# Kernel optimization log

Hardware: AMD Instinct MI355X
Metric: run time of the kernel (lower is better)

Reference implementation:

```python
import jax, jax.numpy as jnp
import numpy as np

B, S, D, H, NH, C = 32, 512, 768, 768, 4, 10
HD = H // NH


def _lin(x, w, b):
    return x @ w.T + b


def _ln(x, g, b, eps=1e-5):
    mu = jnp.mean(x, axis=-1, keepdims=True)
    var = jnp.mean(jnp.square(x - mu), axis=-1, keepdims=True)
    return (x - mu) * jax.lax.rsqrt(var + eps) * g + b


def setup_inputs() -> dict:
    key = jax.random.key(0)
    ks = jax.random.split(key, 16)
    w = lambda k, shape: jax.random.normal(k, shape, dtype=jnp.float32) * 0.02
    return {
        "x": jax.random.normal(ks[0], (B, S, D), dtype=jnp.float32),
        "wq": w(ks[1], (H, D)), "bq": jnp.zeros((H,), jnp.float32),
        "wk": w(ks[2], (H, D)), "bk": jnp.zeros((H,), jnp.float32),
        "wv": w(ks[3], (H, D)), "bv": jnp.zeros((H,), jnp.float32),
        "wx": w(ks[4], (H, D)), "bx": jnp.zeros((H,), jnp.float32),
        "in_proj_w": w(ks[5], (3 * H, H)), "in_proj_b": jnp.zeros((3 * H,), jnp.float32),
        "out_proj_w": w(ks[6], (H, H)), "out_proj_b": jnp.zeros((H,), jnp.float32),
        "fc1a_w": w(ks[7], (H, H)), "fc1a_b": jnp.zeros((H,), jnp.float32),
        "fc1b_w": w(ks[8], (H, H)), "fc1b_b": jnp.zeros((H,), jnp.float32),
        "ln_g": jnp.ones((H,), jnp.float32), "ln_b": jnp.zeros((H,), jnp.float32),
        "fc2_w": w(ks[9], (C, H)), "fc2_b": jnp.zeros((C,), jnp.float32),
    }


def reference(x, wq, bq, wk, bk, wv, bv, wx, bx, in_proj_w, in_proj_b,
              out_proj_w, out_proj_b, fc1a_w, fc1a_b, fc1b_w, fc1b_b,
              ln_g, ln_b, fc2_w, fc2_b):
    # Vectorized sinusoidal PE matching the triple loop:
    # even i: sin(pos / 10000^(2i/D)); odd i: cos(pos / 10000^(2(i-1)/D))
    d = x.shape[2]
    pos = jnp.arange(x.shape[1], dtype=x.dtype)[:, None]          # [S,1]
    i = jnp.arange(d)
    i_even = (i - (i % 2)).astype(x.dtype)                        # 2*(i - i%2)/d exponent
    angle = pos / jnp.power(jnp.asarray(10000.0, x.dtype), 2.0 * i_even / d)  # [S,D]
    pe = jnp.where(i % 2 == 0, jnp.sin(angle), jnp.cos(angle))
    x = x + pe[None]

    q = _lin(x, wq, bq)
    k = _lin(x, wk, bk)
    v = _lin(x, wv, bv)
    xr = _lin(x, wx, bx)

    # torch MultiheadAttention: in_proj, split heads, SDPA, out_proj
    wq_i, wk_i, wv_i = jnp.split(in_proj_w, 3, axis=0)
    bq_i, bk_i, bv_i = jnp.split(in_proj_b, 3, axis=0)
    b = x.shape[0]
    q2 = _lin(q, wq_i, bq_i).reshape(b, -1, NH, HD)
    k2 = _lin(k, wk_i, bk_i).reshape(b, -1, NH, HD)
    v2 = _lin(v, wv_i, bv_i).reshape(b, -1, NH, HD)
    scores = jnp.einsum('bqhd,bkhd->bhqk', q2, k2) / jnp.sqrt(jnp.asarray(HD, x.dtype))
    attn = jax.nn.softmax(scores, axis=-1)
    ctx = jnp.einsum('bhqk,bkhd->bqhd', attn, v2).reshape(b, -1, H)
    attn_out = _lin(ctx, out_proj_w, out_proj_b)

    x = _ln(xr + attn_out, ln_g, ln_b)
    ffn = _lin(jax.nn.relu(_lin(x, fc1a_w, fc1a_b)), fc1b_w, fc1b_b)
    x = _ln(x + ffn, ln_g, ln_b)
    x = jnp.sum(x, axis=1)
    return _lin(x, fc2_w, fc2_b)
```

## Files before the change

kernel.cpp:

```cpp
#include <hip/hip_runtime.h>
#include <hip/hip_bf16.h>

typedef __bf16 bf16;
typedef __bf16 bf16x8 __attribute__((ext_vector_type(8)));
typedef __bf16 bf16x4 __attribute__((ext_vector_type(4)));
typedef __bf16 bf16x2 __attribute__((ext_vector_type(2)));
typedef float  f32x4  __attribute__((ext_vector_type(4)));

#define GLD16(g, l) __builtin_amdgcn_global_load_lds(                        \
    (const __attribute__((address_space(1))) void*)(g),                      \
    (__attribute__((address_space(3))) void*)(l), 16, 0, 0)

template<int BM, int BN, int MFR, int NFR>
__global__ __launch_bounds__(256, 3)
void gemm_nt(const bf16* __restrict__ A, const bf16* __restrict__ B,
             bf16* __restrict__ C, const float* __restrict__ bias,
             int K, int lda, int ldb, int ldc,
             int inner,
             long long aOut, long long aIn,
             long long bOut, long long bIn,
             long long cOut, long long cIn,
             float alpha, int relu,
             const bf16* __restrict__ res, int ldr)
{
    const int z  = blockIdx.z;
    const int zo = z / inner;
    const int zi = z - zo * inner;
    A += (long long)zo * aOut + (long long)zi * aIn;
    B += (long long)zo * bOut + (long long)zi * bIn;
    C += (long long)zo * cOut + (long long)zi * cIn;

    const int tm = blockIdx.y * BM;
    const int tn = blockIdx.x * BN;

    __shared__ __align__(16) bf16 smem[(BM + BN) * 64];
    bf16* As = smem;
    bf16* Bs = smem + BM * 64;

    const int tid  = threadIdx.x;
    const int lane = tid & 63;
    const int wid  = tid >> 6;
    const int wr   = wid >> 1;
    const int wc   = wid & 1;

    f32x4 acc[MFR][NFR];
#pragma unroll
    for (int i = 0; i < MFR; ++i)
#pragma unroll
        for (int j = 0; j < NFR; ++j) acc[i][j] = (f32x4){0.f, 0.f, 0.f, 0.f};

    const int srow = lane >> 3;
    const int gch8 = ((lane & 7) ^ srow) * 8;

    const int NA = BM / 32;
    const int NB = BN / 32;

    const bf16* aP[NA];
#pragma unroll
    for (int jj = 0; jj < NA; ++jj) {
        const int R0 = (wid * NA + jj) * 8;
        aP[jj] = A + (long long)(tm + R0 + srow) * lda + gch8;
    }
    const bf16* bP[NB];
#pragma unroll
    for (int jj = 0; jj < NB; ++jj) {
        const int R0 = (wid * NB + jj) * 8;
        bP[jj] = B + (long long)(tn + R0 + srow) * ldb + gch8;
    }

    const int lr = lane & 15;
    const int qg = lane >> 4;

    for (int kt = 0; kt < K; kt += 64) {
#pragma unroll
        for (int jj = 0; jj < NA; ++jj)
            GLD16(aP[jj], As + (wid * NA + jj) * 512);
#pragma unroll
        for (int jj = 0; jj < NB; ++jj)
            GLD16(bP[jj], Bs + (wid * NB + jj) * 512);
        __syncthreads();

#pragma unroll
        for (int h = 0; h < 2; ++h) {
            const int off = ((qg + h * 4) ^ (lr & 7)) * 8;
            bf16x8 af[MFR], bfr[NFR];
#pragma unroll
            for (int i = 0; i < MFR; ++i)
                af[i] = *(const bf16x8*)(As + (wr * MFR * 16 + i * 16 + lr) * 64 + off);
#pragma unroll
            for (int j = 0; j < NFR; ++j)
                bfr[j] = *(const bf16x8*)(Bs + (wc * NFR * 16 + j * 16 + lr) * 64 + off);
#pragma unroll
            for (int i = 0; i < MFR; ++i)
#pragma unroll
                for (int j = 0; j < NFR; ++j)
                    acc[i][j] = __builtin_amdgcn_mfma_f32_16x16x32_bf16(
                        af[i], bfr[j], acc[i][j], 0, 0, 0);
        }
        __syncthreads();
#pragma unroll
        for (int jj = 0; jj < NA; ++jj) aP[jj] += 64;
#pragma unroll
        for (int jj = 0; jj < NB; ++jj) bP[jj] += 64;
    }

#pragma unroll
    for (int i = 0; i < MFR; ++i) {
#pragma unroll
        for (int j = 0; j < NFR; ++j) {
            const int mm0 = tm + wr * MFR * 16 + i * 16 + (lane >> 4) * 4;
            const int nn  = tn + wc * NFR * 16 + j * 16 + (lane & 15);
#pragma unroll
            for (int r = 0; r < 4; ++r) {
                float v = acc[i][j][r] * alpha;
                if (bias) v += bias[nn];
                if (res)  v += (float)res[(long long)(mm0 + r) * ldr + nn];
                if (relu) v = fmaxf(v, 0.f);
                C[(long long)(mm0 + r) * ldc + nn] = (bf16)v;
            }
        }
    }
}

#define BAR8()  __builtin_amdgcn_s_barrier()
#define LGKM0() do { asm volatile("s_waitcnt lgkmcnt(0)" ::: "memory");      \
                     __builtin_amdgcn_sched_barrier(0); } while (0)

#define RD_A(S, MB)                                                          \
    _Pragma("unroll") for (int mi = 0; mi < 4; ++mi)                         \
    _Pragma("unroll") for (int h = 0; h < 2; ++h)                            \
        af[mi][h] = *(const bf16x8*)((S) + aBase + ((MB) + mi) * 1024 +      \
                                     (h ? koff1 : koff0));

#define RD_B(S, NJ)                                                          \
    _Pragma("unroll") for (int h = 0; h < 2; ++h)                            \
        bfv[NJ][h] = *(const bf16x8*)((S) + bBase + (NJ) * 1024 +            \
                                      (h ? koff1 : koff0));

#define MFMA_Q(MB, N0, N1)                                                   \
    __builtin_amdgcn_s_setprio(1);                                          \
    _Pragma("unroll") for (int h = 0; h < 2; ++h)                            \
    _Pragma("unroll") for (int mi = 0; mi < 4; ++mi) {                       \
        acc[(MB)+mi][(N0)] = __builtin_amdgcn_mfma_f32_16x16x32_bf16(        \
            af[mi][h], bfv[(N0)][h], acc[(MB)+mi][(N0)], 0, 0, 0);           \
        acc[(MB)+mi][(N1)] = __builtin_amdgcn_mfma_f32_16x16x32_bf16(        \
            af[mi][h], bfv[(N1)][h], acc[(MB)+mi][(N1)], 0, 0, 0);           \
    }                                                                        \
    __builtin_amdgcn_s_setprio(0);

#define STAGE_A(DST)                                                         \
    _Pragma("unroll") for (int jj = 0; jj < 4; ++jj) {                       \
        GLD16(aP[jj], (DST) + (wid * 4 + jj) * 512);  aP[jj] += 64; }

#define STAGE_B(DST)                                                         \
    _Pragma("unroll") for (int jj = 0; jj < 4; ++jj) {                       \
        GLD16(bP[jj], (DST) + 16384 + (wid * 4 + jj) * 512);  bP[jj] += 64; }

#define K_TILE_F(CUR, NXT, STG, LAST)                                        \
  {                                                                          \
    RD_A((CUR), 0); RD_B((CUR), 0); RD_B((CUR), 1);                          \
    if (STG) { STAGE_A(NXT) }                                                \
    LGKM0();                                                                 \
    MFMA_Q(0, 0, 1)                                                          \
    RD_B((CUR), 2); RD_B((CUR), 3);                                          \
    if (STG) { STAGE_B(NXT) }                                                \
    LGKM0();                                                                 \
    MFMA_Q(0, 2, 3)                                                          \
    RD_A((CUR), 4);                                                          \
    LGKM0();                                                                 \
    MFMA_Q(4, 2, 3)                                                          \
    MFMA_Q(4, 0, 1)                                                          \
    if (!(LAST)) { asm volatile("s_waitcnt vmcnt(0)" ::: "memory");          \
                   __builtin_amdgcn_sched_barrier(0); BAR8(); }              \
  }

__global__ __launch_bounds__(512, 2)
void gemm_qkv_8ph(const bf16* __restrict__ A, const bf16* __restrict__ B,
                  bf16* __restrict__ C, const float* __restrict__ bias)
{
    constexpr int LDA = 768, LDB = 768, LDC = 3072;
    const int tm = blockIdx.y * 256;
    const int tn = blockIdx.x * 256;

    __shared__ __align__(16) bf16 smem[2][2 * 256 * 64];

    const int tid  = threadIdx.x;
    const int lane = tid & 63;
    const int wid  = tid >> 6;
    const int wr   = wid >> 2;
    const int wc   = wid & 3;
    const int lr   = lane & 15;
    const int qg   = lane >> 4;

    const int srow = lane >> 3;
    const int gch8 = ((lane & 7) ^ srow) * 8;
    const bf16* aP[4];
    const bf16* bP[4];
#pragma unroll
    for (int jj = 0; jj < 4; ++jj) {
        aP[jj] = A + (long long)(tm + wid * 32 + jj * 8 + srow) * LDA + gch8;
        bP[jj] = B + (long long)(tn + wid * 32 + jj * 8 + srow) * LDB + gch8;
    }

    f32x4 acc[8][4];
#pragma unroll
    for (int i = 0; i < 8; ++i)
#pragma unroll
        for (int j = 0; j < 4; ++j) acc[i][j] = (f32x4){0.f, 0.f, 0.f, 0.f};

    const int aBase = (wr * 128 + lr) * 64;
    const int bBase = 16384 + (wc * 64 + lr) * 64;
    const int koff0 = ((qg    ) ^ (lr & 7)) * 8;
    const int koff1 = ((qg + 4) ^ (lr & 7)) * 8;

    bf16x8 af[4][2];
    bf16x8 bfv[4][2];

    bf16* S0 = &smem[0][0];
    bf16* S1 = &smem[1][0];

    STAGE_A(S0)
    STAGE_B(S0)
    asm volatile("s_waitcnt vmcnt(0)" ::: "memory");
    BAR8();

#pragma unroll 1
    for (int it = 0; it < 5; ++it) {
        K_TILE_F(S0, S1, 1, 0)
        K_TILE_F(S1, S0, 1, 0)
    }
    K_TILE_F(S0, S1, 1, 0)
    K_TILE_F(S1, S0, 0, 1)

    float bv[4];
#pragma unroll
    for (int j = 0; j < 4; ++j) bv[j] = bias[tn + wc * 64 + j * 16 + lr];

#pragma unroll
    for (int i = 0; i < 8; ++i) {
        const int mm0 = tm + wr * 128 + i * 16 + qg * 4;
#pragma unroll
        for (int j = 0; j < 4; ++j) {
            const int nn = tn + wc * 64 + j * 16 + lr;
#pragma unroll
            for (int r = 0; r < 4; ++r)
                C[(long long)(mm0 + r) * LDC + nn] = (bf16)(acc[i][j][r] + bv[j]);
        }
    }
}

__global__ __launch_bounds__(512, 2)
void gemm_flow(const bf16* __restrict__ A, const bf16* __restrict__ B,
               bf16* __restrict__ C, const float* __restrict__ bias,
               int lda, int ldb, int ldc, int relu,
               const bf16* __restrict__ res, int ldr)
{
    const int tm = blockIdx.y * 256;
    const int tn = blockIdx.x * 256;

    __shared__ __align__(16) bf16 smem[2][2 * 256 * 64];

    const int tid  = threadIdx.x;
    const int lane = tid & 63;
    const int wid  = tid >> 6;
    const int wr   = wid >> 2;
    const int wc   = wid & 3;
    const int lr   = lane & 15;
    const int qg   = lane >> 4;

    const int srow = lane >> 3;
    const int gch8 = ((lane & 7) ^ srow) * 8;
    const bf16* aP[4];
    const bf16* bP[4];
#pragma unroll
    for (int jj = 0; jj < 4; ++jj) {
        aP[jj] = A + (long long)(tm + wid * 32 + jj * 8 + srow) * lda + gch8;
        bP[jj] = B + (long long)(tn + wid * 32 + jj * 8 + srow) * ldb + gch8;
    }

    f32x4 acc[8][4];
#pragma unroll
    for (int i = 0; i < 8; ++i)
#pragma unroll
        for (int j = 0; j < 4; ++j) acc[i][j] = (f32x4){0.f, 0.f, 0.f, 0.f};

    const int aBase = (wr * 128 + lr) * 64;
    const int bBase = 16384 + (wc * 64 + lr) * 64;
    const int koff0 = ((qg    ) ^ (lr & 7)) * 8;
    const int koff1 = ((qg + 4) ^ (lr & 7)) * 8;

    bf16x8 af[4][2];
    bf16x8 bfv[4][2];

    bf16* S0 = &smem[0][0];
    bf16* S1 = &smem[1][0];

    STAGE_A(S0)
    STAGE_B(S0)
    asm volatile("s_waitcnt vmcnt(0)" ::: "memory");
    BAR8();

#pragma unroll 1
    for (int it = 0; it < 5; ++it) {
        K_TILE_F(S0, S1, 1, 0)
        K_TILE_F(S1, S0, 1, 0)
    }
    K_TILE_F(S0, S1, 1, 0)
    K_TILE_F(S1, S0, 0, 1)

    float bv[4];
#pragma unroll
    for (int j = 0; j < 4; ++j) bv[j] = bias ? bias[tn + wc * 64 + j * 16 + lr] : 0.f;

#pragma unroll
    for (int i = 0; i < 8; ++i) {
        const int mm0 = tm + wr * 128 + i * 16 + qg * 4;
#pragma unroll
        for (int j = 0; j < 4; ++j) {
            const int nn = tn + wc * 64 + j * 16 + lr;
#pragma unroll
            for (int r = 0; r < 4; ++r) {
                float v = acc[i][j][r] + bv[j];
                if (res)  v += (float)res[(long long)(mm0 + r) * ldr + nn];
                if (relu) v = fmaxf(v, 0.f);
                C[(long long)(mm0 + r) * ldc + nn] = (bf16)v;
            }
        }
    }
}

__global__ __launch_bounds__(256, 2)
void fused_attn_kernel(bf16* __restrict__ qkvx)
{
    const int flat = blockIdx.x;
    const int qt = (flat >> 3) & 3;
    const int z  = (flat & 7) | ((flat >> 5) << 3);
    const int b  = z >> 2, h = z & 3;

    const bf16* Qg = qkvx + (long long)b * 512 * 3072 + h * 192;
    const bf16* Kg = Qg + 768;
    const bf16* Vg = Qg + 1536;

    __shared__ __align__(16) bf16 Ks[64 * 192];
    __shared__ __align__(16) bf16 VTs[192 * 64];
    __shared__ __align__(16) bf16 Pb[4 * 32 * 64];

    const int tid  = threadIdx.x;
    const int lane = tid & 63;
    const int wid  = tid >> 6;
    const int lr   = lane & 15;
    const int qg   = lane >> 4;
    const int m0   = qt * 128 + wid * 32;

    bf16x8 qf[2][6];
#pragma unroll
    for (int mt = 0; mt < 2; ++mt)
#pragma unroll
        for (int t = 0; t < 6; ++t)
            qf[mt][t] = *(const bf16x8*)(Qg + (long long)(m0 + mt * 16 + lr) * 3072
                                         + t * 32 + qg * 8);

    const bf16* kP[6];
#pragma unroll
    for (int i = 0; i < 6; ++i) {
        const int c = i * 256 + tid;
        const int krow = c / 24, kcc = c % 24;
        const int kgc  = (kcc & 24) | ((kcc & 7) ^ (krow & 7));
        kP[i] = Kg + (long long)krow * 3072 + kgc * 8;
    }
    const int vkp = tid & 31;
    const int vdc = tid >> 5;

    f32x4 acc[2][12];
#pragma unroll
    for (int mt = 0; mt < 2; ++mt)
#pragma unroll
        for (int dt = 0; dt < 12; ++dt) acc[mt][dt] = (f32x4){0.f, 0.f, 0.f, 0.f};
    float mrow[2][4], lrow[2][4];
#pragma unroll
    for (int mt = 0; mt < 2; ++mt)
#pragma unroll
        for (int r = 0; r < 4; ++r) { mrow[mt][r] = -3e38f; lrow[mt][r] = 0.f; }

    const float alpha = 0.0721687836f;

    for (int kt = 0; kt < 8; ++kt) {
#pragma unroll
        for (int i = 0; i < 6; ++i)
            GLD16(kP[i], Ks + (i * 256 + wid * 64) * 8);
#pragma unroll
        for (int i = 0; i < 3; ++i) {
            const int dc = vdc + i * 8;
            const bf16* p = Vg + (long long)(2 * vkp) * 3072 + dc * 8;
            const bf16x8 v0 = *(const bf16x8*)(p);
            const bf16x8 v1 = *(const bf16x8*)(p + 3072);
#pragma unroll
            for (int j = 0; j < 8; ++j) {
                const int d = dc * 8 + j;
                bf16x2 pk; pk[0] = v0[j]; pk[1] = v1[j];
                *(bf16x2*)(VTs + d * 64 + ((vkp >> 2) ^ (d & 7)) * 8
                           + 2 * (vkp & 3)) = pk;
            }
        }
        __syncthreads();

        f32x4 sf[2][4];
#pragma unroll
        for (int mt = 0; mt < 2; ++mt)
#pragma unroll
            for (int nt = 0; nt < 4; ++nt) sf[mt][nt] = (f32x4){0.f, 0.f, 0.f, 0.f};
#pragma unroll
        for (int nt = 0; nt < 4; ++nt) {
#pragma unroll
            for (int t = 0; t < 6; ++t) {
                const int ch = t * 4 + qg;
                const int ph = (ch & 24) | ((ch & 7) ^ (lr & 7));
                const bf16x8 kf = *(const bf16x8*)(Ks + (nt * 16 + lr) * 192 + ph * 8);
                sf[0][nt] = __builtin_amdgcn_mfma_f32_16x16x32_bf16(qf[0][t], kf, sf[0][nt], 0, 0, 0);
                sf[1][nt] = __builtin_amdgcn_mfma_f32_16x16x32_bf16(qf[1][t], kf, sf[1][nt], 0, 0, 0);
            }
        }

#pragma unroll
        for (int mt = 0; mt < 2; ++mt) {
            float mx[4], a[4], rs[4], p[4][4];
#pragma unroll
            for (int r = 0; r < 4; ++r) {
                float v0 = fmaxf(sf[mt][0][r], sf[mt][1][r]);
                float v1 = fmaxf(sf[mt][2][r], sf[mt][3][r]);
                mx[r] = fmaxf(v0, v1) * alpha;
            }
#pragma unroll
            for (int msk = 1; msk <= 8; msk <<= 1)
#pragma unroll
                for (int r = 0; r < 4; ++r) mx[r] = fmaxf(mx[r], __shfl_xor(mx[r], msk));
#pragma unroll
            for (int r = 0; r < 4; ++r) {
                const float mn = fmaxf(mrow[mt][r], mx[r]);
                a[r] = __expf(mrow[mt][r] - mn);
                mrow[mt][r] = mn;
                rs[r] = 0.f;
            }
#pragma unroll
            for (int nt = 0; nt < 4; ++nt)
#pragma unroll
                for (int r = 0; r < 4; ++r) {
                    p[nt][r] = __expf(sf[mt][nt][r] * alpha - mrow[mt][r]);
                    rs[r] += p[nt][r];
                }
#pragma unroll
            for (int msk = 1; msk <= 8; msk <<= 1)
#pragma unroll
                for (int r = 0; r < 4; ++r) rs[r] += __shfl_xor(rs[r], msk);
#pragma unroll
            for (int r = 0; r < 4; ++r) lrow[mt][r] = lrow[mt][r] * a[r] + rs[r];
#pragma unroll
            for (int dt = 0; dt < 12; ++dt)
#pragma unroll
                for (int r = 0; r < 4; ++r) acc[mt][dt][r] *= a[r];
#pragma unroll
            for (int nt = 0; nt < 4; ++nt)
#pragma unroll
                for (int r = 0; r < 4; ++r) {
                    const int row = mt * 16 + qg * 4 + r;
                    const int ph2 = (nt * 2 + (lr >> 3)) ^ (row & 7);
                    Pb[wid * 2048 + row * 64 + ph2 * 8 + (lr & 7)] = (bf16)p[nt][r];
                }
        }

        bf16x8 pf[2][2];
#pragma unroll
        for (int mt = 0; mt < 2; ++mt)
#pragma unroll
            for (int ks = 0; ks < 2; ++ks) {
                const int row = mt * 16 + lr;
                const int ph  = (ks * 4 + qg) ^ (lr & 7);
                pf[mt][ks] = *(const bf16x8*)(Pb + wid * 2048 + row * 64 + ph * 8);
            }
#pragma unroll
        for (int dt = 0; dt < 12; ++dt) {
#pragma unroll
            for (int ks = 0; ks < 2; ++ks) {
                const int ph = (ks * 4 + qg) ^ (lr & 7);
                const bf16x8 vf = *(const bf16x8*)(VTs + (dt * 16 + lr) * 64 + ph * 8);
                acc[0][dt] = __builtin_amdgcn_mfma_f32_16x16x32_bf16(pf[0][ks], vf, acc[0][dt], 0, 0, 0);
                acc[1][dt] = __builtin_amdgcn_mfma_f32_16x16x32_bf16(pf[1][ks], vf, acc[1][dt], 0, 0, 0);
            }
        }
        __syncthreads();
#pragma unroll
        for (int i = 0; i < 6; ++i) kP[i] += 64 * 3072;
        Vg += 64 * 3072;
    }

    bf16* Og = qkvx + (long long)b * 512 * 3072 + h * 192;
#pragma unroll
    for (int mt = 0; mt < 2; ++mt) {
        float inv[4];
#pragma unroll
        for (int r = 0; r < 4; ++r) inv[r] = 1.0f / lrow[mt][r];
#pragma unroll
        for (int dt = 0; dt < 12; ++dt)
#pragma unroll
            for (int r = 0; r < 4; ++r) {
                const int row = m0 + mt * 16 + qg * 4 + r;
                Og[(long long)row * 3072 + dt * 16 + lr] = (bf16)(acc[mt][dt][r] * inv[r]);
            }
    }
}

__device__ __forceinline__ void cast4(const float* src, bf16* dst, int i)
{
    const float4 v = *(const float4*)(src + (long long)i * 4);
    bf16x4 o;
    o[0] = (bf16)v.x; o[1] = (bf16)v.y; o[2] = (bf16)v.z; o[3] = (bf16)v.w;
    *(bf16x4*)(dst + (long long)i * 4) = o;
}

__global__ __launch_bounds__(256)
void prep_kernel(const float* __restrict__ wq, const float* __restrict__ wk,
                 const float* __restrict__ wv, const float* __restrict__ wx,
                 const float* __restrict__ inpw, const float* __restrict__ inpb,
                 const float* __restrict__ bq, const float* __restrict__ bk,
                 const float* __restrict__ bv, const float* __restrict__ bx,
                 const float* __restrict__ woutp, const float* __restrict__ wf1a,
                 const float* __restrict__ wf1b, const float* __restrict__ x,
                 bf16* __restrict__ WT3, bf16* __restrict__ INPJ,
                 bf16* __restrict__ WOUT, bf16* __restrict__ WF1A,
                 bf16* __restrict__ WF1B, bf16* __restrict__ WXD,
                 float* __restrict__ BCAT, bf16* __restrict__ XPE)
{
    const int blk = blockIdx.x;
    const int tid = threadIdx.x;
    __shared__ bf16 t[32][33];

    if (blk < 1728) {
        const int which = blk / 576, local = blk - which * 576;
        const float* src = (which == 0) ? wq : ((which == 1) ? wk : wv);
        bf16* dst = WT3 + (long long)which * 589824;
        const int r0 = (local / 24) * 32, c0 = (local % 24) * 32;
        const int tr = tid >> 5, tc = tid & 31;
#pragma unroll
        for (int k = 0; k < 4; ++k) {
            const int r = tr + k * 8;
            t[r][tc] = (bf16)src[(long long)(r0 + r) * 768 + c0 + tc];
        }
        __syncthreads();
#pragma unroll
        for (int k = 0; k < 4; ++k) {
            const int c = tr + k * 8;
            dst[(long long)(c0 + c) * 768 + r0 + tc] = t[tc][c];
        }
    } else if (blk < 3456) {
        cast4(inpw, INPJ, (blk - 1728) * 256 + tid);
    } else if (blk < 4032) {
        cast4(woutp, WOUT, (blk - 3456) * 256 + tid);
    } else if (blk < 4608) {
        cast4(wf1a, WF1A, (blk - 4032) * 256 + tid);
    } else if (blk < 5184) {
        cast4(wf1b, WF1B, (blk - 4608) * 256 + tid);
    } else if (blk < 5760) {
        cast4(wx, WXD, (blk - 5184) * 256 + tid);
    } else if (blk < 6051) {
        const int bl = blk - 5760;
        if (bl < 288) {
            const int g = tid >> 5, l = tid & 31;
            const int n = bl * 8 + g;
            const int zsec = n / 768;
            const float* bb = (zsec == 0) ? bq : ((zsec == 1) ? bk : bv);
            const float* wrow = inpw + (long long)n * 768;
            float s = 0.f;
            for (int d = l; d < 768; d += 32) s += wrow[d] * bb[d];
#pragma unroll
            for (int off = 16; off; off >>= 1) s += __shfl_xor(s, off);
            if (l == 0) BCAT[n] = inpb[n] + s;
        } else {
            const int n = (bl - 288) * 256 + tid;
            if (n < 768) BCAT[2304 + n] = bx[n];
        }
    } else {
        const int idx4 = ((blk - 6051) * 256 + tid) * 4;
        const int d    = idx4 % 768;
        const int row  = idx4 / 768;
        const int s    = row & 511;
        const float ksc = -0.034603417655076f;
        const float4 xv = *(const float4*)(x + (long long)idx4);
        float a0 = (float)s * exp2f((float)d * ksc);
        float a1 = (float)s * exp2f((float)(d + 2) * ksc);
        float s0, c0, s1, c1;
        sincosf(a0, &s0, &c0);
        sincosf(a1, &s1, &c1);
        bf16x4 o;
        o[0] = (bf16)(xv.x + s0);
        o[1] = (bf16)(xv.y + c0);
        o[2] = (bf16)(xv.z + s1);
        o[3] = (bf16)(xv.w + c1);
        *(bf16x4*)(XPE + (long long)idx4) = o;
    }
}

__global__ __launch_bounds__(192)
void ln1_kernel(const bf16* __restrict__ a, int lda_,
                bf16* __restrict__ o, int ldo,
                const float* __restrict__ g, const float* __restrict__ be)
{
    const int row = blockIdx.x;
    const int t   = threadIdx.x;
    const int d0  = t * 4;
    const bf16x4 av = *(const bf16x4*)(a + (long long)row * lda_ + d0);
    float xv[4];
#pragma unroll
    for (int k = 0; k < 4; ++k) xv[k] = (float)av[k];
    float s1 = xv[0] + xv[1] + xv[2] + xv[3];
    float s2 = xv[0]*xv[0] + xv[1]*xv[1] + xv[2]*xv[2] + xv[3]*xv[3];
    for (int off = 32; off; off >>= 1) {
        s1 += __shfl_xor(s1, off);
        s2 += __shfl_xor(s2, off);
    }
    __shared__ float red[6];
    const int wid = t >> 6, lane = t & 63;
    if (lane == 0) { red[wid] = s1; red[3 + wid] = s2; }
    __syncthreads();
    s1 = red[0] + red[1] + red[2];
    s2 = red[3] + red[4] + red[5];
    const float mu  = s1 * (1.0f / 768.0f);
    const float var = s2 * (1.0f / 768.0f) - mu * mu;
    const float rs  = rsqrtf(var + 1e-5f);
    const float4 gv = *(const float4*)(g + d0);
    const float4 ev = *(const float4*)(be + d0);
    bf16x4 ov;
    ov[0] = (bf16)(((xv[0] - mu) * rs) * gv.x + ev.x);
    ov[1] = (bf16)(((xv[1] - mu) * rs) * gv.y + ev.y);
    ov[2] = (bf16)(((xv[2] - mu) * rs) * gv.z + ev.z);
    ov[3] = (bf16)(((xv[3] - mu) * rs) * gv.w + ev.w);
    *(bf16x4*)(o + (long long)row * ldo + d0) = ov;
}

__global__ __launch_bounds__(256)
void ln2_reduce_kernel(const bf16* __restrict__ src,
                       const float* __restrict__ g, const float* __restrict__ be,
                       float* __restrict__ partial)
{
    const int blk  = blockIdx.x;
    const int tid  = threadIdx.x;
    const int wid  = tid >> 6, lane = tid & 63;
    const int d0   = lane * 12;

    float gv[12], ev[12];
#pragma unroll
    for (int k = 0; k < 12; k += 4) {
        *(float4*)(gv + k) = *(const float4*)(g + d0 + k);
        *(float4*)(ev + k) = *(const float4*)(be + d0 + k);
    }
    float acc[12];
#pragma unroll
    for (int k = 0; k < 12; ++k) acc[k] = 0.f;

    for (int i = 0; i < 8; ++i) {
        const int row = blk * 32 + i * 4 + wid;
        const bf16* p = src + (long long)row * 3072 + d0;
        float xv[12];
#pragma unroll
        for (int k = 0; k < 12; k += 4) {
            const bf16x4 v = *(const bf16x4*)(p + k);
            xv[k] = (float)v[0]; xv[k+1] = (float)v[1];
            xv[k+2] = (float)v[2]; xv[k+3] = (float)v[3];
        }
        float s1 = 0.f, s2 = 0.f;
#pragma unroll
        for (int k = 0; k < 12; ++k) { s1 += xv[k]; s2 += xv[k] * xv[k]; }
        for (int off = 32; off; off >>= 1) {
            s1 += __shfl_xor(s1, off);
            s2 += __shfl_xor(s2, off);
        }
        const float mu  = s1 * (1.0f / 768.0f);
        const float var = s2 * (1.0f / 768.0f) - mu * mu;
        const float rs  = rsqrtf(var + 1e-5f);
#pragma unroll
        for (int k = 0; k < 12; ++k) acc[k] += (xv[k] - mu) * rs * gv[k] + ev[k];
    }

    __shared__ float red[4][768];
#pragma unroll
    for (int k = 0; k < 12; k += 4)
        *(float4*)(&red[wid][d0 + k]) = *(const float4*)(acc + k);
    __syncthreads();
    if (wid == 0) {
#pragma unroll
        for (int k = 0; k < 12; k += 4) {
            const float4 a0 = *(const float4*)(&red[0][d0 + k]);
            const float4 a1 = *(const float4*)(&red[1][d0 + k]);
            const float4 a2 = *(const float4*)(&red[2][d0 + k]);
            const float4 a3 = *(const float4*)(&red[3][d0 + k]);
            *(float4*)(partial + (long long)blk * 768 + d0 + k) =
                make_float4(a0.x + a1.x + a2.x + a3.x, a0.y + a1.y + a2.y + a3.y,
                            a0.z + a1.z + a2.z + a3.z, a0.w + a1.w + a2.w + a3.w);
        }
    }
}

__global__ __launch_bounds__(192)
void reduce_fc2_stage2_kernel(const float* __restrict__ partial, const float* __restrict__ w,
                              const float* __restrict__ bias, float* __restrict__ out)
{
    const int b = blockIdx.x, t = threadIdx.x;
    const int d0 = t * 4;
    float a[4] = {0.f, 0.f, 0.f, 0.f};
    for (int c = 0; c < 16; ++c) {
        const float4 pv = *(const float4*)(partial + (long long)(b * 16 + c) * 768 + d0);
        a[0] += pv.x; a[1] += pv.y; a[2] += pv.z; a[3] += pv.w;
    }
    __shared__ float os[10];
    if (t < 10) os[t] = 0.f;
    __syncthreads();
    for (int c = 0; c < 10; ++c) {
        const float4 wv = *(const float4*)(w + c * 768 + d0);
        float p = wv.x * a[0] + wv.y * a[1] + wv.z * a[2] + wv.w * a[3];
        for (int off = 32; off; off >>= 1) p += __shfl_xor(p, off);
        if ((t & 63) == 0) atomicAdd(&os[c], p);
    }
    __syncthreads();
    if (t < 10) out[b * 10 + t] = os[t] + bias[t];
}

static const size_t OFF_XPE  = 0;
static const size_t OFF_WCAT = OFF_XPE  + (size_t)16384 * 768 * 2;
static const size_t OFF_WT3  = OFF_WCAT + (size_t)3072 * 768 * 2;
static const size_t OFF_INPJ = OFF_WT3  + (size_t)3 * 768 * 768 * 2;
static const size_t OFF_WOUT = OFF_INPJ + (size_t)2304 * 768 * 2;
static const size_t OFF_WF1A = OFF_WOUT + (size_t)768 * 768 * 2;
static const size_t OFF_WF1B = OFF_WF1A + (size_t)768 * 768 * 2;
static const size_t OFF_BCAT = OFF_WF1B + (size_t)768 * 768 * 2;
static const size_t OFF_QKVX = OFF_BCAT + (size_t)3072 * 4;
static const size_t OFF_VT   = OFF_QKVX + (size_t)16384 * 3072 * 2;
static const size_t OFF_S    = OFF_VT   + (size_t)128 * 192 * 512 * 2;
static const size_t OFF_X1   = OFF_S    + (size_t)128 * 512 * 512 * 2;

extern "C" void kernel_launch(void* const* d_in, const int* in_sizes, int n_in,
                              void* d_out, int out_size, void* d_ws, size_t ws_size,
                              hipStream_t stream)
{
    const float* x     = (const float*)d_in[0];
    const float* wq    = (const float*)d_in[1];
    const float* bq    = (const float*)d_in[2];
    const float* wk    = (const float*)d_in[3];
    const float* bk    = (const float*)d_in[4];
    const float* wv    = (const float*)d_in[5];
    const float* bv    = (const float*)d_in[6];
    const float* wx    = (const float*)d_in[7];
    const float* bx    = (const float*)d_in[8];
    const float* inpw  = (const float*)d_in[9];
    const float* inpb  = (const float*)d_in[10];
    const float* woutp = (const float*)d_in[11];
    const float* boutp = (const float*)d_in[12];
    const float* wf1a  = (const float*)d_in[13];
    const float* bf1a  = (const float*)d_in[14];
    const float* wf1b  = (const float*)d_in[15];
    const float* bf1b  = (const float*)d_in[16];
    const float* lng   = (const float*)d_in[17];
    const float* lnb   = (const float*)d_in[18];
    const float* wfc2  = (const float*)d_in[19];
    const float* bfc2  = (const float*)d_in[20];
    float* out = (float*)d_out;

    char* ws = (char*)d_ws;
    bf16*  XPE  = (bf16*)(ws + OFF_XPE);
    bf16*  WCAT = (bf16*)(ws + OFF_WCAT);
    bf16*  WT3  = (bf16*)(ws + OFF_WT3);
    bf16*  INPJ = (bf16*)(ws + OFF_INPJ);
    bf16*  WOUT = (bf16*)(ws + OFF_WOUT);
    bf16*  WF1A = (bf16*)(ws + OFF_WF1A);
    bf16*  WF1B = (bf16*)(ws + OFF_WF1B);
    float* BCAT = (float*)(ws + OFF_BCAT);
    bf16*  QKVX = (bf16*)(ws + OFF_QKVX);
    float* PART = (float*)(ws + OFF_S);
    bf16*  X1   = (bf16*)(ws + OFF_X1);

    prep_kernel<<<18339, 256, 0, stream>>>(wq, wk, wv, wx, inpw, inpb,
                                           bq, bk, bv, bx, woutp, wf1a, wf1b, x,
                                           WT3, INPJ, WOUT, WF1A, WF1B,
                                           WCAT + (size_t)2304 * 768, BCAT, XPE);

    gemm_nt<64, 128, 2, 4><<<dim3(6, 12, 3), 256, 0, stream>>>(
        INPJ, WT3, WCAT, nullptr, 768, 768, 768, 768,
        1, 589824, 0, 589824, 0, 589824, 0, 1.0f, 0, nullptr, 0);

    gemm_qkv_8ph<<<dim3(12, 64, 1), 512, 0, stream>>>(XPE, WCAT, QKVX, BCAT);

    fused_attn_kernel<<<512, 256, 0, stream>>>(QKVX);

    gemm_flow<<<dim3(3, 64, 1), 512, 0, stream>>>(
        QKVX, WOUT, QKVX + 768, boutp, 3072, 768, 3072,
        0, QKVX + 2304, 3072);

    ln1_kernel<<<16384, 192, 0, stream>>>(QKVX + 768, 3072, X1, 768, lng, lnb);

    gemm_flow<<<dim3(3, 64, 1), 512, 0, stream>>>(
        X1, WF1A, QKVX + 1536, bf1a, 768, 768, 3072,
        1, nullptr, 0);

    gemm_flow<<<dim3(3, 64, 1), 512, 0, stream>>>(
        QKVX + 1536, WF1B, QKVX + 2304, bf1b, 3072, 768, 3072,
        0, X1, 768);

    ln2_reduce_kernel<<<512, 256, 0, stream>>>(QKVX + 2304, lng, lnb, PART);

    reduce_fc2_stage2_kernel<<<32, 192, 0, stream>>>(PART, wfc2, bfc2, out);
}
```

Baseline: 455.2 us.

## Prefetch next K/V tiles into registers during attention compute

The attention kernel now loads the next K and V tiles from global memory into registers right after the barrier, so those loads overlap with the QK^T, softmax and PV MFMA work of the current tile. The direct global-to-LDS loads for K are replaced by register stores to LDS. Full __syncthreads are swapped for explicit lgkmcnt waits, raw barriers and sched_barriers so the compiler cannot sink the prefetch past the compute. The cost is more vector registers (kreg and vreg) on top of an already large accumulator set, which may lower occupancy or cause spills.

```diff
diff --git a/kernel.cpp b/kernel.cpp
--- a/kernel.cpp
+++ b/kernel.cpp
@@ -370,6 +370,18 @@
     }
     const int vkp = tid & 31;
     const int vdc = tid >> 5;
+    const bf16* vB = Vg + (long long)(2 * vkp) * 3072;
+
+    bf16x8 kreg[6];
+    bf16x8 vreg[3][2];
+#pragma unroll
+    for (int i = 0; i < 6; ++i) kreg[i] = *(const bf16x8*)kP[i];
+#pragma unroll
+    for (int i = 0; i < 3; ++i) {
+        const bf16* p = vB + (vdc + i * 8) * 8;
+        vreg[i][0] = *(const bf16x8*)(p);
+        vreg[i][1] = *(const bf16x8*)(p + 3072);
+    }
 
     f32x4 acc[2][12];
 #pragma unroll
@@ -387,22 +399,37 @@
     for (int kt = 0; kt < 8; ++kt) {
 #pragma unroll
         for (int i = 0; i < 6; ++i)
-            GLD16(kP[i], Ks + (i * 256 + wid * 64) * 8);
+            *(bf16x8*)(Ks + (i * 256 + wid * 64 + lane) * 8) = kreg[i];
 #pragma unroll
         for (int i = 0; i < 3; ++i) {
             const int dc = vdc + i * 8;
-            const bf16* p = Vg + (long long)(2 * vkp) * 3072 + dc * 8;
-            const bf16x8 v0 = *(const bf16x8*)(p);
-            const bf16x8 v1 = *(const bf16x8*)(p + 3072);
 #pragma unroll
             for (int j = 0; j < 8; ++j) {
                 const int d = dc * 8 + j;
-                bf16x2 pk; pk[0] = v0[j]; pk[1] = v1[j];
+                bf16x2 pk; pk[0] = vreg[i][0][j]; pk[1] = vreg[i][1][j];
                 *(bf16x2*)(VTs + d * 64 + ((vkp >> 2) ^ (d & 7)) * 8
                            + 2 * (vkp & 3)) = pk;
             }
         }
-        __syncthreads();
+        asm volatile("s_waitcnt lgkmcnt(0)" ::: "memory");
+        __builtin_amdgcn_s_barrier();
+        __builtin_amdgcn_sched_barrier(0);
+
+        if (kt < 7) {
+#pragma unroll
+            for (int i = 0; i < 6; ++i) {
+                kP[i] += 64 * 3072;
+                kreg[i] = *(const bf16x8*)kP[i];
+            }
+            vB += 64 * 3072;
+#pragma unroll
+            for (int i = 0; i < 3; ++i) {
+                const bf16* p = vB + (vdc + i * 8) * 8;
+                vreg[i][0] = *(const bf16x8*)(p);
+                vreg[i][1] = *(const bf16x8*)(p + 3072);
+            }
+        }
+        __builtin_amdgcn_sched_barrier(0);
 
         f32x4 sf[2][4];
 #pragma unroll
@@ -487,10 +514,9 @@
                 acc[1][dt] = __builtin_amdgcn_mfma_f32_16x16x32_bf16(pf[1][ks], vf, acc[1][dt], 0, 0, 0);
             }
         }
-        __syncthreads();
-#pragma unroll
-        for (int i = 0; i < 6; ++i) kP[i] += 64 * 3072;
-        Vg += 64 * 3072;
+        asm volatile("s_waitcnt lgkmcnt(0)" ::: "memory");
+        __builtin_amdgcn_s_barrier();
+        __builtin_amdgcn_sched_barrier(0);
     }
 
     bf16* Og = qkvx + (long long)b * 512 * 3072 + h * 192;
```

Result: slower. 554.5 us (+21.8%).
